# Kernel tuning notes

Hardware: AMD Instinct MI355X
Metric: run time of the kernel (lower is better)

## Reference

```python
import jax, jax.numpy as jnp
import numpy as np
from jax.scipy.linalg import expm

N_QUBITS = 13
N_LAYERS = 4  # ceil(log2(13))


def _apply_2axes(T, M, a0, a1):
    """Apply 4x4 matrix M to the pair of 2-dim axes (a0, a1) of tensor T."""
    nd = T.ndim
    T = jnp.moveaxis(T, (a0, a1), (nd - 2, nd - 1))
    s = T.shape
    T = (T.reshape(s[:-2] + (4,)) @ M.T).reshape(s)
    return jnp.moveaxis(T, (nd - 2, nd - 1), (a0, a1))


def _conv_pairs(n):
    pairs = [(2 * i, 2 * i + 1) for i in range(n // 2)]
    if n > 2:
        pairs += [(2 * i + 1, (2 * i + 2) % n) for i in range(n // 2)]
    return pairs


def _conv_state(psi, U, n):
    # psi: [B] + [2]*n pure state
    for q0, q1 in _conv_pairs(n):
        psi = _apply_2axes(psi, U, 1 + q0, 1 + q1)
    return psi


def _conv_dm(rho, U, n):
    # rho: [B] + [2]*n (rows) + [2]*n (cols); apply U on rows, U* on cols
    Uc = U.conj()
    for q0, q1 in _conv_pairs(n):
        rho = _apply_2axes(rho, U, 1 + q0, 1 + q1)
        rho = _apply_2axes(rho, Uc, 1 + n + q0, 1 + n + q1)
    return rho


def _pool_dm(rho, n):
    # measure-and-discard qubits 0..n//2-1 (with index shifting these are the
    # original even-indexed qubits); averaging over outcomes == partial trace.
    measured = [2 * i for i in range(n // 2)]
    cur = n
    for q in reversed(measured):  # descending so lower indices stay valid
        rho = jnp.trace(rho, axis1=1 + q, axis2=1 + cur + q)
        cur -= 1
    return rho, cur


def setup_inputs() -> dict:
    key = jax.random.key(0)
    k1, k2, k3, k4 = jax.random.split(key, 4)
    B, D = 2, 2 ** N_QUBITS
    return {
        "psi_real": jax.random.normal(k1, (B, D), dtype=jnp.float32),
        "psi_imag": jax.random.normal(k2, (B, D), dtype=jnp.float32),
        "H_real": jax.random.normal(k3, (N_LAYERS, 4, 4), dtype=jnp.float32),
        "H_imag": jax.random.normal(k4, (N_LAYERS, 4, 4), dtype=jnp.float32),
    }


def reference(psi_real, psi_imag, H_real, H_imag):
    B = psi_real.shape[0]
    n = N_QUBITS
    psi = (psi_real + 1j * psi_imag).astype(jnp.complex64)
    psi = psi / jnp.linalg.norm(psi, axis=1, keepdims=True)
    H = (H_real + 1j * H_imag).astype(jnp.complex64)
    # anti-hermitian generator -> unitary gate per layer
    Us = [expm(H[i] - H[i].conj().T) for i in range(N_LAYERS)]

    # layer 0: conv on pure state, then convert to density matrix, then pool
    psi = psi.reshape((B,) + (2,) * n)
    psi = _conv_state(psi, Us[0], n)
    flat = psi.reshape(B, -1)
    rho = (flat[:, :, None] * flat[:, None, :].conj()).reshape((B,) + (2,) * (2 * n))
    rho, n = _pool_dm(rho, n)

    for i in range(1, N_LAYERS):
        rho = _conv_dm(rho, Us[i], n)
        rho, n = _pool_dm(rho, n)

    # n == 1 here: measure qubit 0, return P(outcome 0)
    rho = rho.reshape(B, 2, 2)
    return rho[:, 0, 0].real
```

## Files before the change

kernel.cpp:

```cpp
#include <hip/hip_runtime.h>


#define NT 256
#define HDIM 4096

typedef float v2f __attribute__((ext_vector_type(2)));

__device__ __forceinline__ float2 cadds(float2 a, float2 b) {
    return make_float2(a.x + b.x, a.y + b.y);
}
__device__ __forceinline__ float2 cmacs(float2 acc, float2 a, float2 b) {
    acc.x = fmaf(a.x, b.x, fmaf(-a.y, b.y, acc.x));
    acc.y = fmaf(a.x, b.y, fmaf(a.y, b.x, acc.y));
    return acc;
}
__device__ __forceinline__ float2 shflc(float2 v, int src) {
    return make_float2(__shfl(v.x, src, 64), __shfl(v.y, src, 64));
}

__device__ __forceinline__ v2f cma(v2f acc, v2f u, v2f us, v2f a) {
#pragma clang fp contract(fast)
    v2f ax = __builtin_shufflevector(a, a, 0, 0);
    v2f ay = __builtin_shufflevector(a, a, 1, 1);
    acc = ax * u + acc;
    acc = ay * us + acc;
    return acc;
}

__device__ float2 expm_compute(float are, float aim) {
    const int lane = threadIdx.x & 63;
    const int e = lane & 15, r = e >> 2, c = e & 3;
    const int base = lane & 48;

    float v = fabsf(are) + fabsf(aim);
    v += __shfl_xor(v, 1, 64);
    v += __shfl_xor(v, 2, 64);
    v = fmaxf(v, __shfl_xor(v, 4, 64));
    v = fmaxf(v, __shfl_xor(v, 8, 64));
    v = fmaxf(v, __shfl_xor(v, 16, 64));
    v = fmaxf(v, __shfl_xor(v, 32, 64));

    int s = 0;
    while (v > 0.25f && s < 30) { v *= 0.5f; s++; }
    const float scale = ldexpf(1.0f, -s);

    float2 X = make_float2(are * scale, aim * scale);
    float2 E = X;
    if (r == c) E.x += 1.0f;
    float2 T = X;
    for (int k = 2; k <= 10; k++) {
        float2 acc = make_float2(0.f, 0.f);
        #pragma unroll
        for (int kk = 0; kk < 4; kk++) {
            float2 t = shflc(T, base + r * 4 + kk);
            float2 x = shflc(X, base + kk * 4 + c);
            acc = cmacs(acc, t, x);
        }
        const float inv = 1.0f / (float)k;
        T = make_float2(acc.x * inv, acc.y * inv);
        E = cadds(E, T);
    }
    for (int i = 0; i < s; i++) {
        float2 acc = make_float2(0.f, 0.f);
        #pragma unroll
        for (int kk = 0; kk < 4; kk++) {
            float2 a = shflc(E, base + r * 4 + kk);
            float2 bb = shflc(E, base + kk * 4 + c);
            acc = cmacs(acc, a, bb);
        }
        E = acc;
    }
    return E;
}

__device__ __forceinline__ void loadU(float2 E, int L, v2f* u, v2f* us) {
    #pragma unroll
    for (int k = 0; k < 16; k++) {
        float ur = __shfl(E.x, (L << 4) | k, 64);
        float ui = __shfl(E.y, (L << 4) | k, 64);
        u[k] = (v2f){ur, ui};
        us[k] = (v2f){-ui, ur};
    }
}

__device__ __forceinline__ int swz(int e) {
    return e ^ ((e >> 4) & 15) ^ ((e >> 8) & 15);
}

template<int MASK>
__device__ __forceinline__ int deposit(int t) {
    int r = 0;
    #pragma unroll
    for (int p = 0; p < 12; p++) {
        if (MASK & (1 << p)) { r |= (t & 1) << p; t >>= 1; }
    }
    return r;
}

template<int B3, int B2, int B1, int B0>
__device__ __forceinline__ int eaddr4(int base, int i) {
    return base | (((i >> 3) & 1) << B3) | (((i >> 2) & 1) << B2)
                | (((i >> 1) & 1) << B1) | ((i & 1) << B0);
}

template<int B3, int B2, int B1, int B0, int MASK>
__device__ __forceinline__ void phase_read(v2f* v, const v2f* psi, int t) {
    const int base = deposit<MASK>(t);
    #pragma unroll
    for (int i = 0; i < 16; i++) v[i] = psi[swz(eaddr4<B3, B2, B1, B0>(base, i))];
}
template<int B3, int B2, int B1, int B0, int MASK>
__device__ __forceinline__ void phase_write(const v2f* v, v2f* psi, int t) {
    const int base = deposit<MASK>(t);
    #pragma unroll
    for (int i = 0; i < 16; i++) psi[swz(eaddr4<B3, B2, B1, B0>(base, i))] = v[i];
}

template<int KA, int KB>
__device__ __forceinline__ void apply_gate(v2f* v, const v2f* u, const v2f* us) {
    const int MA = 1 << KA, MB = 1 << KB;
    #pragma unroll
    for (int i = 0; i < 16; i++) {
        if (i & (MA | MB)) continue;
        v2f a0 = v[i], a1 = v[i | MB], a2 = v[i | MA], a3 = v[i | MA | MB];
        v2f z = {0.f, 0.f};
        v2f n0 = cma(cma(cma(cma(z, u[0], us[0], a0), u[1], us[1], a1),
                         u[2], us[2], a2), u[3], us[3], a3);
        v2f n1 = cma(cma(cma(cma(z, u[4], us[4], a0), u[5], us[5], a1),
                         u[6], us[6], a2), u[7], us[7], a3);
        v2f n2 = cma(cma(cma(cma(z, u[8], us[8], a0), u[9], us[9], a1),
                         u[10], us[10], a2), u[11], us[11], a3);
        v2f n3 = cma(cma(cma(cma(z, u[12], us[12], a0), u[13], us[13], a1),
                         u[14], us[14], a2), u[15], us[15], a3);
        v[i] = n0; v[i | MB] = n1; v[i | MA] = n2; v[i | MA | MB] = n3;
    }
}

__global__ __launch_bounds__(NT, 1) void qcnn_kernel(
    const float* __restrict__ pr, const float* __restrict__ pi,
    const float* __restrict__ Hr, const float* __restrict__ Hi,
    float* __restrict__ out) {
    __shared__ v2f psi[HDIM];
    const int t = threadIdx.x;
    const int b = blockIdx.x >> 1;
    const int h = blockIdx.x & 1;
    const int lane = t & 63;
    const int m = lane >> 4, ee = lane & 15, r = ee >> 2, c = ee & 3;

    float hra = Hr[m * 16 + r * 4 + c], hrb = Hr[m * 16 + c * 4 + r];
    float hia = Hi[m * 16 + r * 4 + c], hib = Hi[m * 16 + c * 4 + r];

    const float* prb = pr + b * 2 * HDIM;
    const float* pib = pi + b * 2 * HDIM;
    v2f w[32];
    #pragma unroll
    for (int i = 0; i < 32; i++) {
        int g = (((i >> 4) & 1) << 12) | (((i >> 3) & 1) << 11)
              | (((i >> 2) & 1) << 10) | (((i >> 1) & 1) << 9)
              | ((i & 1) << 8) | t;
        w[i] = (v2f){prb[g], pib[g]};
    }

    float2 E = expm_compute(hra - hrb, hia + hib);

    float norm2 = 0.f;
    #pragma unroll
    for (int i = 0; i < 32; i++)
        norm2 = fmaf(w[i].x, w[i].x, fmaf(w[i].y, w[i].y, norm2));

    v2f u[16], us[16];
    loadU(E, 0, u, us);

    v2f v[16];
    #pragma unroll
    for (int i = 0; i < 8; i++) {
        v2f a0 = w[i], a1 = w[i | 8], a2 = w[i | 16], a3 = w[i | 24];
        v2f z = {0.f, 0.f};
        v2f lo, hi;
        if (h == 0) {
            lo = cma(cma(cma(cma(z, u[0], us[0], a0), u[1], us[1], a1),
                         u[2], us[2], a2), u[3], us[3], a3);
            hi = cma(cma(cma(cma(z, u[4], us[4], a0), u[5], us[5], a1),
                         u[6], us[6], a2), u[7], us[7], a3);
        } else {
            lo = cma(cma(cma(cma(z, u[8], us[8], a0), u[9], us[9], a1),
                         u[10], us[10], a2), u[11], us[11], a3);
            hi = cma(cma(cma(cma(z, u[12], us[12], a0), u[13], us[13], a1),
                         u[14], us[14], a2), u[15], us[15], a3);
        }
        v[i] = lo; v[i | 8] = hi;
    }
    apply_gate<2, 1>(v, u, us);
    apply_gate<3, 2>(v, u, us);
    phase_write<11, 10, 9, 8, 0x0FF>(v, psi, t);
    __syncthreads();

    phase_read<8, 7, 6, 5, 0xE1F>(v, psi, t);
    apply_gate<3, 2>(v, u, us);
    apply_gate<1, 0>(v, u, us);
    apply_gate<2, 1>(v, u, us);
    phase_write<8, 7, 6, 5, 0xE1F>(v, psi, t);
    __syncthreads();

    phase_read<4, 3, 2, 1, 0xFE1>(v, psi, t);
    apply_gate<3, 2>(v, u, us);
    apply_gate<1, 0>(v, u, us);
    apply_gate<2, 1>(v, u, us);
    phase_write<4, 3, 2, 1, 0xFE1>(v, psi, t);
    __syncthreads();

    phase_read<9, 8, 5, 4, 0xCCF>(v, psi, t);
    apply_gate<3, 2>(v, u, us);
    apply_gate<1, 0>(v, u, us);
    phase_write<9, 8, 5, 4, 0xCCF>(v, psi, t);
    __syncthreads();

    phase_read<11, 9, 1, 0, 0x5FC>(v, psi, t);
    apply_gate<1, 0>(v, u, us);
    loadU(E, 1, u, us);
    apply_gate<3, 2>(v, u, us);
    phase_write<11, 9, 1, 0, 0x5FC>(v, psi, t);
    __syncthreads();

    phase_read<7, 5, 3, 1, 0xF55>(v, psi, t);
    apply_gate<3, 2>(v, u, us);
    apply_gate<1, 0>(v, u, us);
    apply_gate<2, 1>(v, u, us);
    phase_write<7, 5, 3, 1, 0xF55>(v, psi, t);
    __syncthreads();

    phase_read<9, 7, 1, 0, 0xD7C>(v, psi, t);
    apply_gate<3, 2>(v, u, us);
    apply_gate<1, 0>(v, u, us);
    loadU(E, 2, u, us);
    apply_gate<1, 0>(v, u, us);
    phase_write<9, 7, 1, 0, 0xD7C>(v, psi, t);
    __syncthreads();

    phase_read<9, 5, 1, 0, 0xDDC>(v, psi, t);
    apply_gate<3, 2>(v, u, us);
    apply_gate<2, 1>(v, u, us);
    apply_gate<0, 3>(v, u, us);
    loadU(E, 3, u, us);
    apply_gate<2, 0>(v, u, us);

    float s0 = 0.f;
    #pragma unroll
    for (int i = 0; i < 16; i += 2)
        s0 = fmaf(v[i].x, v[i].x, fmaf(v[i].y, v[i].y, s0));

    #pragma unroll
    for (int off = 1; off < 64; off <<= 1) {
        s0 += __shfl_xor(s0, off, 64);
        norm2 += __shfl_xor(norm2, off, 64);
    }
    __syncthreads();
    if (lane == 0) psi[t >> 6] = (v2f){s0, norm2};
    __syncthreads();
    if (t == 0) {
        float S = 0.f, Nrm = 0.f;
        #pragma unroll
        for (int wv = 0; wv < NT / 64; wv++) { S += psi[wv].x; Nrm += psi[wv].y; }
        atomicAdd(&out[b], S / Nrm);
    }
}

extern "C" void kernel_launch(void* const* d_in, const int* in_sizes, int n_in,
                              void* d_out, int out_size, void* d_ws, size_t ws_size,
                              hipStream_t stream) {
    const float* pr = (const float*)d_in[0];
    const float* pi = (const float*)d_in[1];
    const float* Hr = (const float*)d_in[2];
    const float* Hi = (const float*)d_in[3];
    float* out = (float*)d_out;
    hipMemsetAsync(out, 0, out_size * sizeof(float), stream);
    qcnn_kernel<<<dim3(out_size * 2), dim3(NT), 0, stream>>>(pr, pi, Hr, Hi, out);
}
```

Measured before the change: 72.92 us.

## Split each batch element across four blocks by fixing a second qubit

Each batch element's work is now split over four workgroups instead of two, fixing a second high-order qubit index (bit 8) per block in addition to the existing split. The later conv/pool phases then work on 8 amplitudes per thread with 3-qubit gate helpers, and the phase sequence is rebuilt for the new qubit ordering. This roughly halves per-block shared-memory and ALU work so more CUs run in parallel, at the cost of redundant global loads and duplicated early gate work in every block, plus more atomic adds.

```diff
diff --git a/kernel.cpp b/kernel.cpp
--- a/kernel.cpp
+++ b/kernel.cpp
@@ -102,6 +102,11 @@
     return base | (((i >> 3) & 1) << B3) | (((i >> 2) & 1) << B2)
                 | (((i >> 1) & 1) << B1) | ((i & 1) << B0);
 }
+template<int B2, int B1, int B0>
+__device__ __forceinline__ int eaddr3(int base, int i) {
+    return base | (((i >> 2) & 1) << B2) | (((i >> 1) & 1) << B1)
+                | ((i & 1) << B0);
+}
 
 template<int B3, int B2, int B1, int B0, int MASK>
 __device__ __forceinline__ void phase_read(v2f* v, const v2f* psi, int t) {
@@ -114,6 +119,19 @@
     const int base = deposit<MASK>(t);
     #pragma unroll
     for (int i = 0; i < 16; i++) psi[swz(eaddr4<B3, B2, B1, B0>(base, i))] = v[i];
+}
+
+template<int B2, int B1, int B0, int MASK>
+__device__ __forceinline__ void q_read(v2f* q, const v2f* psi, int t, int hb8) {
+    const int base = deposit<MASK>(t) | hb8;
+    #pragma unroll
+    for (int i = 0; i < 8; i++) q[i] = psi[swz(eaddr3<B2, B1, B0>(base, i))];
+}
+template<int B2, int B1, int B0, int MASK>
+__device__ __forceinline__ void q_write(const v2f* q, v2f* psi, int t, int hb8) {
+    const int base = deposit<MASK>(t) | hb8;
+    #pragma unroll
+    for (int i = 0; i < 8; i++) psi[swz(eaddr3<B2, B1, B0>(base, i))] = q[i];
 }
 
 template<int KA, int KB>
@@ -135,6 +153,25 @@
         v[i] = n0; v[i | MB] = n1; v[i | MA] = n2; v[i | MA | MB] = n3;
     }
 }
+template<int KA, int KB>
+__device__ __forceinline__ void apply_gate3(v2f* v, const v2f* u, const v2f* us) {
+    const int MA = 1 << KA, MB = 1 << KB;
+    #pragma unroll
+    for (int i = 0; i < 8; i++) {
+        if (i & (MA | MB)) continue;
+        v2f a0 = v[i], a1 = v[i | MB], a2 = v[i | MA], a3 = v[i | MA | MB];
+        v2f z = {0.f, 0.f};
+        v2f n0 = cma(cma(cma(cma(z, u[0], us[0], a0), u[1], us[1], a1),
+                         u[2], us[2], a2), u[3], us[3], a3);
+        v2f n1 = cma(cma(cma(cma(z, u[4], us[4], a0), u[5], us[5], a1),
+                         u[6], us[6], a2), u[7], us[7], a3);
+        v2f n2 = cma(cma(cma(cma(z, u[8], us[8], a0), u[9], us[9], a1),
+                         u[10], us[10], a2), u[11], us[11], a3);
+        v2f n3 = cma(cma(cma(cma(z, u[12], us[12], a0), u[13], us[13], a1),
+                         u[14], us[14], a2), u[15], us[15], a3);
+        v[i] = n0; v[i | MB] = n1; v[i | MA] = n2; v[i | MA | MB] = n3;
+    }
+}
 
 __global__ __launch_bounds__(NT, 1) void qcnn_kernel(
     const float* __restrict__ pr, const float* __restrict__ pi,
@@ -142,8 +179,10 @@
     float* __restrict__ out) {
     __shared__ v2f psi[HDIM];
     const int t = threadIdx.x;
-    const int b = blockIdx.x >> 1;
-    const int h = blockIdx.x & 1;
+    const int blk = blockIdx.x;
+    const int b = blk >> 2;
+    const int h12 = (blk >> 1) & 1;
+    const int hb8 = (blk & 1) << 8;
     const int lane = t & 63;
     const int m = lane >> 4, ee = lane & 15, r = ee >> 2, c = ee & 3;
 
@@ -177,7 +216,7 @@
         v2f a0 = w[i], a1 = w[i | 8], a2 = w[i | 16], a3 = w[i | 24];
         v2f z = {0.f, 0.f};
         v2f lo, hi;
-        if (h == 0) {
+        if (h12 == 0) {
             lo = cma(cma(cma(cma(z, u[0], us[0], a0), u[1], us[1], a1),
                          u[2], us[2], a2), u[3], us[3], a3);
             hi = cma(cma(cma(cma(z, u[4], us[4], a0), u[5], us[5], a1),
@@ -195,59 +234,81 @@
     phase_write<11, 10, 9, 8, 0x0FF>(v, psi, t);
     __syncthreads();
 
-    phase_read<8, 7, 6, 5, 0xE1F>(v, psi, t);
+    phase_read<9, 8, 7, 6, 0xC3F>(v, psi, t);
+    apply_gate<2, 1>(v, u, us);
     apply_gate<3, 2>(v, u, us);
-    apply_gate<1, 0>(v, u, us);
-    apply_gate<2, 1>(v, u, us);
-    phase_write<8, 7, 6, 5, 0xE1F>(v, psi, t);
-    __syncthreads();
-
-    phase_read<4, 3, 2, 1, 0xFE1>(v, psi, t);
-    apply_gate<3, 2>(v, u, us);
-    apply_gate<1, 0>(v, u, us);
-    apply_gate<2, 1>(v, u, us);
-    phase_write<4, 3, 2, 1, 0xFE1>(v, psi, t);
-    __syncthreads();
-
-    phase_read<9, 8, 5, 4, 0xCCF>(v, psi, t);
-    apply_gate<3, 2>(v, u, us);
-    apply_gate<1, 0>(v, u, us);
-    phase_write<9, 8, 5, 4, 0xCCF>(v, psi, t);
-    __syncthreads();
-
-    phase_read<11, 9, 1, 0, 0x5FC>(v, psi, t);
-    apply_gate<1, 0>(v, u, us);
+    {
+        const int base2 = deposit<0xC3F>(t);
+        #pragma unroll
+        for (int i = 0; i < 16; i++) {
+            if ((((i >> 2) & 1) << 8) != hb8) continue;
+            psi[swz(base2 | (((i >> 3) & 1) << 9) | (((i >> 2) & 1) << 8)
+                          | (((i >> 1) & 1) << 7) | ((i & 1) << 6))] = v[i];
+        }
+    }
+    __syncthreads();
+
+    v2f q[8];
+
+    q_read<2, 1, 0, 0xEF8>(q, psi, t, hb8);
+    apply_gate3<2, 1>(q, u, us);
+    apply_gate3<1, 0>(q, u, us);
+    q_write<2, 1, 0, 0xEF8>(q, psi, t, hb8);
+    __syncthreads();
+
+    q_read<4, 3, 2, 0xEE3>(q, psi, t, hb8);
+    apply_gate3<2, 1>(q, u, us);
+    apply_gate3<1, 0>(q, u, us);
+    q_write<4, 3, 2, 0xEE3>(q, psi, t, hb8);
+    __syncthreads();
+
+    q_read<6, 5, 4, 0xE8F>(q, psi, t, hb8);
+    apply_gate3<2, 1>(q, u, us);
+    apply_gate3<1, 0>(q, u, us);
+    q_write<6, 5, 4, 0xE8F>(q, psi, t, hb8);
+    __syncthreads();
+
+    q_read<7, 6, 5, 0xE1F>(q, psi, t, hb8);
+    apply_gate3<2, 1>(q, u, us);
     loadU(E, 1, u, us);
-    apply_gate<3, 2>(v, u, us);
-    phase_write<11, 9, 1, 0, 0x5FC>(v, psi, t);
-    __syncthreads();
-
-    phase_read<7, 5, 3, 1, 0xF55>(v, psi, t);
-    apply_gate<3, 2>(v, u, us);
-    apply_gate<1, 0>(v, u, us);
-    apply_gate<2, 1>(v, u, us);
-    phase_write<7, 5, 3, 1, 0xF55>(v, psi, t);
-    __syncthreads();
-
-    phase_read<9, 7, 1, 0, 0xD7C>(v, psi, t);
-    apply_gate<3, 2>(v, u, us);
-    apply_gate<1, 0>(v, u, us);
+    apply_gate3<2, 0>(q, u, us);
+    q_write<7, 6, 5, 0xE1F>(q, psi, t, hb8);
+    __syncthreads();
+
+    q_read<11, 9, 7, 0x47F>(q, psi, t, hb8);
+    apply_gate3<2, 1>(q, u, us);
+    apply_gate3<1, 0>(q, u, us);
+    q_write<11, 9, 7, 0x47F>(q, psi, t, hb8);
+    __syncthreads();
+
+    q_read<5, 3, 1, 0xED5>(q, psi, t, hb8);
+    apply_gate3<1, 0>(q, u, us);
+    apply_gate3<2, 1>(q, u, us);
+    q_write<5, 3, 1, 0xED5>(q, psi, t, hb8);
+    __syncthreads();
+
+    q_read<5, 1, 0, 0xEDC>(q, psi, t, hb8);
+    apply_gate3<1, 0>(q, u, us);
     loadU(E, 2, u, us);
-    apply_gate<1, 0>(v, u, us);
-    phase_write<9, 7, 1, 0, 0xD7C>(v, psi, t);
-    __syncthreads();
-
-    phase_read<9, 5, 1, 0, 0xDDC>(v, psi, t);
-    apply_gate<3, 2>(v, u, us);
-    apply_gate<2, 1>(v, u, us);
-    apply_gate<0, 3>(v, u, us);
+    apply_gate3<1, 0>(q, u, us);
+    q_write<5, 1, 0, 0xEDC>(q, psi, t, hb8);
+    __syncthreads();
+
+    q_read<9, 5, 1, 0xCDD>(q, psi, t, hb8);
+    apply_gate3<2, 1>(q, u, us);
+    apply_gate3<1, 0>(q, u, us);
+    q_write<9, 5, 1, 0xCDD>(q, psi, t, hb8);
+    __syncthreads();
+
+    q_read<9, 5, 0, 0xCDE>(q, psi, t, hb8);
+    apply_gate3<0, 2>(q, u, us);
     loadU(E, 3, u, us);
-    apply_gate<2, 0>(v, u, us);
+    apply_gate3<1, 0>(q, u, us);
 
     float s0 = 0.f;
     #pragma unroll
-    for (int i = 0; i < 16; i += 2)
-        s0 = fmaf(v[i].x, v[i].x, fmaf(v[i].y, v[i].y, s0));
+    for (int i = 0; i < 8; i += 2)
+        s0 = fmaf(q[i].x, q[i].x, fmaf(q[i].y, q[i].y, s0));
 
     #pragma unroll
     for (int off = 1; off < 64; off <<= 1) {
@@ -274,5 +335,5 @@
     const float* Hi = (const float*)d_in[3];
     float* out = (float*)d_out;
     hipMemsetAsync(out, 0, out_size * sizeof(float), stream);
-    qcnn_kernel<<<dim3(out_size * 2), dim3(NT), 0, stream>>>(pr, pi, Hr, Hi, out);
-}
+    qcnn_kernel<<<dim3(out_size * 4), dim3(NT), 0, stream>>>(pr, pi, Hr, Hi, out);
+}
```

Measured after the change: 71.78 us. Within noise of the previous version (-1.6%).
